# Kernel tuning notes

Measured on AMD Instinct MI355X. Metric: run time of the kernel, lower is better.

Reference implementation:

```python
import jax, jax.numpy as jnp
import numpy as np

B, C, E = 4, 2048, 1024
H = 16
HD = E // H  # 64

def setup_inputs() -> dict:
    key = jax.random.key(0)
    k1, k2, k3 = jax.random.split(key, 3)
    x = jax.random.normal(k1, (B, C, E), dtype=jnp.float32)
    W_attn = jax.random.normal(k2, (E, 3 * E), dtype=jnp.float32) * 0.02
    W_proj = jax.random.normal(k3, (E, E), dtype=jnp.float32) * 0.02
    return {"x": x, "W_attn": W_attn, "W_proj": W_proj}

def reference(x, W_attn, W_proj):
    b, c, e = x.shape
    qkv = x @ W_attn                      # [B,C,3E]
    q, k, v = jnp.split(qkv, 3, axis=-1)
    # [B,C,E] -> [B,H,C,HD]
    q = q.reshape(b, c, H, HD).transpose(0, 2, 1, 3)
    k = k.reshape(b, c, H, HD).transpose(0, 2, 1, 3)
    v = v.reshape(b, c, H, HD).transpose(0, 2, 1, 3)
    scale = 1.0 / np.sqrt(HD).astype(np.float32)
    att = jnp.einsum('bhqd,bhkd->bhqk', q, k) * scale  # [B,H,C,C]
    causal = jnp.tril(jnp.ones((c, c), dtype=bool))
    att = jnp.where(causal[None, None, :, :], att, -jnp.inf)
    att = jax.nn.softmax(att, axis=-1)
    y = jnp.einsum('bhqk,bhkd->bhqd', att, v)          # [B,H,C,HD]
    y = y.transpose(0, 2, 1, 3).reshape(b, c, e)
    return y @ W_proj
```

## Files before the change

kernel.cpp:

```cpp
#include <hip/hip_runtime.h>
#include <hip/hip_bf16.h>


typedef unsigned short ushort_t;
typedef __attribute__((ext_vector_type(8))) short short8;
typedef __attribute__((ext_vector_type(4))) float floatx4;
typedef __attribute__((ext_vector_type(16))) float floatx16;
typedef __attribute__((ext_vector_type(2))) unsigned uintx2;

#define NH   16
#define SEQ  2048
#define EMB  1024
#define HDIM 64

#define MFMA32(a, b, c) __builtin_amdgcn_mfma_f32_32x32x16_bf16(a, b, c, 0, 0, 0)
#define WAITVM4() asm volatile("s_waitcnt vmcnt(4)" ::: "memory")
#define WAITVM0() asm volatile("s_waitcnt vmcnt(0)" ::: "memory")

__device__ __forceinline__ ushort_t f2bf(float f) {
    union { float f; unsigned u; } v; v.f = f;
    unsigned r = (v.u + 0x7fffu + ((v.u >> 16) & 1u)) >> 16;
    return (ushort_t)r;
}

__device__ __forceinline__ unsigned cvtpk(float lo, float hi) {
    unsigned r;
    asm("v_cvt_pk_bf16_f32 %0, %1, %2" : "=v"(r) : "v"(lo), "v"(hi));
    return r;
}

__device__ __forceinline__ uintx2 pl32(unsigned a, unsigned b) {
    return __builtin_amdgcn_permlane32_swap(a, b, false, false);
}

__device__ __forceinline__ short8 mk8(unsigned a, unsigned b, unsigned c, unsigned d) {
    union { unsigned w[4]; short8 s; } t;
    t.w[0] = a; t.w[1] = b; t.w[2] = c; t.w[3] = d;
    return t.s;
}

#if defined(__has_builtin) && __has_builtin(__builtin_amdgcn_global_load_lds)
#define HAS_GLL 1
__device__ __forceinline__ void gload16(const ushort_t* g, ushort_t* l) {
    __builtin_amdgcn_global_load_lds((const __attribute__((address_space(1))) void*)g,
                                     (__attribute__((address_space(3))) void*)l, 16, 0, 0);
}
#else
#define HAS_GLL 0
#endif

__global__ __launch_bounds__(256) void cast_k(const float* __restrict__ in,
                                              ushort_t* __restrict__ out) {
    int i = blockIdx.x * 256 + threadIdx.x;
    float4 v0 = ((const float4*)in)[i * 2];
    float4 v1 = ((const float4*)in)[i * 2 + 1];
    short8 t;
    t[0] = (short)f2bf(v0.x); t[1] = (short)f2bf(v0.y);
    t[2] = (short)f2bf(v0.z); t[3] = (short)f2bf(v0.w);
    t[4] = (short)f2bf(v1.x); t[5] = (short)f2bf(v1.y);
    t[6] = (short)f2bf(v1.z); t[7] = (short)f2bf(v1.w);
    ((short8*)out)[i] = t;
}

__global__ void transpose_cast_k(const float* __restrict__ in, ushort_t* __restrict__ out,
                                 int R, int Cc) {
    __shared__ ushort_t tile[32][33];
    int x  = blockIdx.x * 32 + threadIdx.x;
    int y0 = blockIdx.y * 32;
#pragma unroll
    for (int i = 0; i < 32; i += 8)
        tile[threadIdx.y + i][threadIdx.x] = f2bf(in[(size_t)(y0 + threadIdx.y + i) * Cc + x]);
    __syncthreads();
    int xo = blockIdx.y * 32 + threadIdx.x;
    int yo = blockIdx.x * 32;
#pragma unroll
    for (int i = 0; i < 32; i += 8)
        out[(size_t)(yo + threadIdx.y + i) * R + xo] = tile[threadIdx.x][threadIdx.y + i];
}

__global__ void transpose_v_k(const ushort_t* __restrict__ in, ushort_t* __restrict__ out) {
    __shared__ ushort_t tile[32][33];
    int bh = blockIdx.z;
    int c0 = blockIdx.x * 32, d0 = blockIdx.y * 32;
#pragma unroll
    for (int i = 0; i < 32; i += 8)
        tile[threadIdx.y + i][threadIdx.x] =
            in[((size_t)bh * SEQ + c0 + threadIdx.y + i) * HDIM + d0 + threadIdx.x];
    __syncthreads();
#pragma unroll
    for (int i = 0; i < 32; i += 8)
        out[((size_t)bh * HDIM + d0 + threadIdx.y + i) * SEQ + c0 + threadIdx.x] =
            tile[threadIdx.x][threadIdx.y + i];
}

template<int EPI>
__global__ __launch_bounds__(256) void gemm_bt(const ushort_t* __restrict__ A,
                                               const ushort_t* __restrict__ Bt,
                                               void* __restrict__ O0v,
                                               ushort_t* __restrict__ O1,
                                               ushort_t* __restrict__ O2,
                                               int M, int N, int K) {
    __shared__ __align__(16) ushort_t SMg[2 * 128 * 64];
    ushort_t* As = SMg;
    ushort_t* Bs = SMg + 128 * 64;
    const int tid  = threadIdx.x;
    const int wv   = tid >> 6, lane = tid & 63, quad = lane >> 4, l15 = lane & 15;
    const int wm   = wv >> 1, wn = wv & 1;
    const int bm   = blockIdx.x, bn = blockIdx.y;
    const int lrow = lane >> 3;
    const int kg   = (lane & 7) ^ (lrow & 7);
    const int sw   = l15 & 7;
    const float qsc = (EPI == 1 && bn < 8) ? 0.18033688011112042f : 1.0f;

    floatx4 acc[4][4];
#pragma unroll
    for (int i = 0; i < 4; i++)
#pragma unroll
        for (int j = 0; j < 4; j++) acc[i][j] = (floatx4){0.f, 0.f, 0.f, 0.f};

    for (int kt = 0; kt < K; kt += 64) {
#pragma unroll
        for (int it = 0; it < 4; it++) {
            int r0 = it * 32 + wv * 8;
            const ushort_t* ga = &A [(size_t)(bm * 128 + r0 + lrow) * K + kt + kg * 8];
            const ushort_t* gb = &Bt[(size_t)(bn * 128 + r0 + lrow) * K + kt + kg * 8];
#if HAS_GLL
            gload16(ga, &As[r0 * 64]);
            gload16(gb, &Bs[r0 * 64]);
#else
            *(uint4*)&As[(r0 + lrow) * 64 + (lane & 7) * 8] = *(const uint4*)ga;
            *(uint4*)&Bs[(r0 + lrow) * 64 + (lane & 7) * 8] = *(const uint4*)gb;
#endif
        }
        __syncthreads();
#pragma unroll
        for (int ks = 0; ks < 2; ks++) {
            short8 af[4], bf[4];
#pragma unroll
            for (int i = 0; i < 4; i++)
                af[i] = *(const short8*)&As[(wm * 64 + i * 16 + l15) * 64 + (((ks * 4 + quad) ^ sw) * 8)];
#pragma unroll
            for (int j = 0; j < 4; j++)
                bf[j] = *(const short8*)&Bs[(wn * 64 + j * 16 + l15) * 64 + (((ks * 4 + quad) ^ sw) * 8)];
#pragma unroll
            for (int i = 0; i < 4; i++)
#pragma unroll
                for (int j = 0; j < 4; j++)
                    acc[i][j] = __builtin_amdgcn_mfma_f32_16x16x32_bf16(af[i], bf[j], acc[i][j], 0, 0, 0);
        }
        __syncthreads();
    }

    if (EPI == 0) {
#pragma unroll
        for (int i = 0; i < 4; i++)
#pragma unroll
            for (int j = 0; j < 4; j++)
#pragma unroll
                for (int r = 0; r < 4; r++) {
                    int row = bm * 128 + wm * 64 + i * 16 + quad * 4 + r;
                    int col = bn * 128 + wn * 64 + j * 16 + l15;
                    ((float*)O0v)[(size_t)row * N + col] = acc[i][j][r];
                }
    } else {
        ushort_t* E = SMg;
#pragma unroll
        for (int i = 0; i < 4; i++)
#pragma unroll
            for (int j = 0; j < 4; j++)
#pragma unroll
                for (int r = 0; r < 4; r++) {
                    int lr = wm * 64 + i * 16 + quad * 4 + r;
                    int lc = wn * 64 + j * 16 + l15;
                    E[lr * 128 + (((lc >> 3) ^ (lr & 7)) << 3) + (lc & 7)] =
                        f2bf(acc[i][j][r] * qsc);
                }
        __syncthreads();
#pragma unroll
        for (int k2 = 0; k2 < 8; k2++) {
            int id   = wv * 512 + k2 * 64 + lane;
            int head = id >> 10;
            int lr   = (id >> 3) & 127;
            int g    = id & 7;
            int gg   = (head * 8 + g) ^ (lr & 7);
            uint4 val = *(const uint4*)&E[lr * 128 + gg * 8];
            int row = bm * 128 + lr;
            int col = bn * 128 + head * 64;
            int b = row >> 11, c = row & 2047;
            int which = col >> 10, nn = col & 1023;
            int hh = nn >> 6;
            ushort_t* dst = (which == 0) ? (ushort_t*)O0v : (which == 1) ? O1 : O2;
            *(uint4*)&dst[((size_t)(b * NH + hh) * SEQ + c) * HDIM + g * 8] = val;
        }
    }
}

__device__ __forceinline__ void stage_kv(const ushort_t* __restrict__ Kg,
                                         const ushort_t* __restrict__ Vtg,
                                         ushort_t* Kn, ushort_t* Vn,
                                         int bh, int j, int wv, int lane) {
    const int lrow = lane >> 3;
    const int kgs  = (lane & 7) ^ (lrow & 7);
#pragma unroll
    for (int it = 0; it < 2; it++) {
        int r0 = it * 32 + wv * 8;
        const ushort_t* gk = &Kg [((size_t)bh * SEQ  + j * 64 + r0 + lrow) * HDIM + kgs * 8];
        const ushort_t* gv = &Vtg[((size_t)bh * HDIM + r0 + lrow) * SEQ + j * 64 + kgs * 8];
#if HAS_GLL
        gload16(gk, &Kn[r0 * 64]);
        gload16(gv, &Vn[r0 * 64]);
#else
        *(uint4*)&Kn[(r0 + lrow) * 64 + (lane & 7) * 8] = *(const uint4*)gk;
        *(uint4*)&Vn[(r0 + lrow) * 64 + (lane & 7) * 8] = *(const uint4*)gv;
#endif
    }
}

__global__ __launch_bounds__(256) void attn3_k(const ushort_t* __restrict__ Qg,
                                               const ushort_t* __restrict__ Kg,
                                               const ushort_t* __restrict__ Vtg,
                                               ushort_t* __restrict__ Y) {
    __shared__ __align__(16) ushort_t SM[3 * 8192];
    const int tid  = threadIdx.x;
    const int wv   = tid >> 6, lane = tid & 63;
    const int l31  = lane & 31, hf = lane >> 5;
    const int bh   = blockIdx.x, z = blockIdx.y;
    const int qs7  = l31 & 7;
    const int b = bh >> 4, hh = bh & 15;

    for (int pp = 0; pp < 2; pp++) {
        const int qb = pp ? (15 - z) : z;
        const int qrow0 = qb * 128 + wv * 32;
        const int q_abs = qrow0 + l31;
        const int jmax_w = 2 * qb + (wv >> 1);
        const int nj = 2 * qb + 2;

        short8 qf[4];
        {
            const ushort_t* qp = Qg + ((size_t)bh * SEQ + q_abs) * HDIM + hf * 8;
#pragma unroll
            for (int ks = 0; ks < 4; ks++) qf[ks] = *(const short8*)(qp + ks * 16);
        }

        floatx16 o0, o1;
#pragma unroll
        for (int r = 0; r < 16; r++) { o0[r] = 0.f; o1[r] = 0.f; }
        float l_i = 0.f;

        stage_kv(Kg, Vtg, SM,        SM + 4096,  bh, 0, wv, lane);
        stage_kv(Kg, Vtg, SM + 8192, SM + 12288, bh, 1, wv, lane);
        WAITVM4();
        __builtin_amdgcn_s_barrier();

        int cur = 0, stg = 2;
        for (int j = 0; j < nj; j++) {
            ushort_t* Ks = SM + cur * 8192;
            ushort_t* Vs = Ks + 4096;

            const bool issue = (j + 2 < nj);
            if (issue) {
                ushort_t* Kn = SM + stg * 8192;
                stage_kv(Kg, Vtg, Kn, Kn + 4096, bh, j + 2, wv, lane);
            }

            if (j <= jmax_w) {
                floatx16 s0, s1;
#pragma unroll
                for (int r = 0; r < 16; r++) { s0[r] = 0.f; s1[r] = 0.f; }
                __builtin_amdgcn_s_setprio(1);
#pragma unroll
                for (int ks = 0; ks < 4; ks++) {
                    int slot = ((hf + 2 * ks) ^ qs7) * 8;
                    short8 k0 = *(const short8*)&Ks[l31 * 64 + slot];
                    short8 k1 = *(const short8*)&Ks[(32 + l31) * 64 + slot];
                    s0 = MFMA32(k0, qf[ks], s0);
                    s1 = MFMA32(k1, qf[ks], s1);
                }
                __builtin_amdgcn_s_setprio(0);

                if (j == jmax_w) {
                    const int kb0 = j * 64 + 4 * hf;
#pragma unroll
                    for (int r = 0; r < 16; r++) {
                        int key = kb0 + (r & 3) + 8 * (r >> 2);
                        if (key > q_abs)      s0[r] = -1e30f;
                        if (key + 32 > q_abs) s1[r] = -1e30f;
                    }
                }

                float rs0 = 0.f, rs1 = 0.f;
#pragma unroll
                for (int r = 0; r < 16; r++) {
                    s0[r] = __builtin_amdgcn_exp2f(s0[r]);
                    s1[r] = __builtin_amdgcn_exp2f(s1[r]);
                    rs0 += s0[r]; rs1 += s1[r];
                }
                float rs = rs0 + rs1;
                rs += __shfl_xor(rs, 32);
                l_i += rs;

                unsigned u0[8], u1[8];
#pragma unroll
                for (int g = 0; g < 4; g++) {
                    u0[2 * g]     = cvtpk(s0[4 * g],     s0[4 * g + 1]);
                    u0[2 * g + 1] = cvtpk(s0[4 * g + 2], s0[4 * g + 3]);
                    u1[2 * g]     = cvtpk(s1[4 * g],     s1[4 * g + 1]);
                    u1[2 * g + 1] = cvtpk(s1[4 * g + 2], s1[4 * g + 3]);
                }
                unsigned pw[16];
#pragma unroll
                for (int t = 0; t < 2; t++) {
                    const unsigned* u = t ? u1 : u0;
#pragma unroll
                    for (int p = 0; p < 2; p++) {
#pragma unroll
                        for (int i = 0; i < 2; i++) {
                            uintx2 r = pl32(u[4 * p + i], u[4 * p + 2 + i]);
                            pw[8 * t + 4 * p + i]     = r[0];
                            pw[8 * t + 4 * p + 2 + i] = r[1];
                        }
                    }
                }

                __builtin_amdgcn_s_setprio(1);
#pragma unroll
                for (int ks = 0; ks < 4; ks++) {
                    int slot = ((hf + 2 * ks) ^ qs7) * 8;
                    short8 v0 = *(const short8*)&Vs[l31 * 64 + slot];
                    short8 v1 = *(const short8*)&Vs[(32 + l31) * 64 + slot];
                    short8 pf = mk8(pw[4 * ks], pw[4 * ks + 1], pw[4 * ks + 2], pw[4 * ks + 3]);
                    o0 = MFMA32(v0, pf, o0);
                    o1 = MFMA32(v1, pf, o1);
                }
                __builtin_amdgcn_s_setprio(0);
            }

            if (issue) { WAITVM4(); } else { WAITVM0(); }
            __builtin_amdgcn_s_barrier();
            cur = (cur == 2) ? 0 : cur + 1;
            stg = (stg == 2) ? 0 : stg + 1;
        }

        ushort_t* Ew = SM + wv * 2048;
        float inv = 1.0f / l_i;
#pragma unroll
        for (int g = 0; g < 4; g++) {
            uint2 w0, w1;
            w0.x = cvtpk(o0[g * 4] * inv,     o0[g * 4 + 1] * inv);
            w0.y = cvtpk(o0[g * 4 + 2] * inv, o0[g * 4 + 3] * inv);
            w1.x = cvtpk(o1[g * 4] * inv,     o1[g * 4 + 1] * inv);
            w1.y = cvtpk(o1[g * 4 + 2] * inv, o1[g * 4 + 3] * inv);
            *(uint2*)&Ew[l31 * 64 + ((g       ^ qs7) * 8) + 4 * hf] = w0;
            *(uint2*)&Ew[l31 * 64 + (((4 + g) ^ qs7) * 8) + 4 * hf] = w1;
        }
        const int dg = lane & 7;
#pragma unroll
        for (int sb = 0; sb < 4; sb++) {
            int ql = sb * 8 + (lane >> 3);
            uint4 v = *(const uint4*)&Ew[ql * 64 + ((dg ^ (ql & 7)) * 8)];
            *(uint4*)&Y[((size_t)(b * SEQ + qrow0 + ql)) * EMB + hh * HDIM + dg * 8] = v;
        }
        __syncthreads();
    }
}

extern "C" void kernel_launch(void* const* d_in, const int* in_sizes, int n_in,
                              void* d_out, int out_size, void* d_ws, size_t ws_size,
                              hipStream_t stream) {
    const float* x      = (const float*)d_in[0];
    const float* W_attn = (const float*)d_in[1];
    const float* W_proj = (const float*)d_in[2];

    char* ws = (char*)d_ws;
    ushort_t* Wt_attn = (ushort_t*)(ws);
    ushort_t* Wt_proj = (ushort_t*)(ws + 6291456);
    ushort_t* Xb      = (ushort_t*)(ws + 8388608);
    ushort_t* Vt      = Xb;
    ushort_t* Qb      = (ushort_t*)(ws + 25165824);
    ushort_t* Kb      = (ushort_t*)(ws + 41943040);
    ushort_t* Vb      = (ushort_t*)(ws + 58720256);
    ushort_t* Yb      = Vb;

    cast_k<<<4096, 256, 0, stream>>>(x, Xb);
    transpose_cast_k<<<dim3(3072 / 32, 1024 / 32), dim3(32, 8), 0, stream>>>(W_attn, Wt_attn, 1024, 3072);
    transpose_cast_k<<<dim3(1024 / 32, 1024 / 32), dim3(32, 8), 0, stream>>>(W_proj, Wt_proj, 1024, 1024);
    gemm_bt<1><<<dim3(8192 / 128, 3072 / 128), 256, 0, stream>>>(Xb, Wt_attn, Qb, Kb, Vb, 8192, 3072, 1024);
    transpose_v_k<<<dim3(SEQ / 32, HDIM / 32, 64), dim3(32, 8), 0, stream>>>(Vb, Vt);
    attn3_k<<<dim3(64, 8), 256, 0, stream>>>(Qb, Kb, Vt, Yb);
    gemm_bt<0><<<dim3(8192 / 128, 1024 / 128), 256, 0, stream>>>(Yb, Wt_proj, d_out,
                                                                 nullptr, nullptr, 8192, 1024, 1024);
}
```

Measured before the change: 254.6 us.

## Rewrite QKV GEMM with 256x256 double-buffered tiles and fuse V transpose

Replaces the templated QKV GEMM with a dedicated 512-thread kernel. It uses 256x256 output tiles, double-buffered LDS staging interleaved with MFMA phases, and a swizzled block order meant to improve L2 reuse. The epilogue writes V directly in transposed layout, which removes the separate transpose_v_k launch and its extra global round trip. In exchange it uses 128KB of shared memory per block, a larger accumulator footprint, and a gathered scalar LDS read pattern for the V transpose that may be bank-conflicted.

Result: slower. 268.4 us (+5.4%).

```diff
diff --git a/kernel.cpp b/kernel.cpp
--- a/kernel.cpp
+++ b/kernel.cpp
@@ -14,7 +14,9 @@
 #define HDIM 64
 
 #define MFMA32(a, b, c) __builtin_amdgcn_mfma_f32_32x32x16_bf16(a, b, c, 0, 0, 0)
+#define MFMA16(a, b, c) __builtin_amdgcn_mfma_f32_16x16x32_bf16(a, b, c, 0, 0, 0)
 #define WAITVM4() asm volatile("s_waitcnt vmcnt(4)" ::: "memory")
+#define WAITVM2() asm volatile("s_waitcnt vmcnt(2)" ::: "memory")
 #define WAITVM0() asm volatile("s_waitcnt vmcnt(0)" ::: "memory")
 
 __device__ __forceinline__ ushort_t f2bf(float f) {
@@ -47,6 +49,10 @@
 }
 #else
 #define HAS_GLL 0
+__device__ __forceinline__ void gload16(const ushort_t* g, ushort_t* l) {
+    int lane = threadIdx.x & 63;
+    *(uint4*)(l + lane * 8) = *(const uint4*)g;
+}
 #endif
 
 __global__ __launch_bounds__(256) void cast_k(const float* __restrict__ in,
@@ -78,31 +84,183 @@
         out[(size_t)(yo + threadIdx.y + i) * R + xo] = tile[threadIdx.x][threadIdx.y + i];
 }
 
-__global__ void transpose_v_k(const ushort_t* __restrict__ in, ushort_t* __restrict__ out) {
-    __shared__ ushort_t tile[32][33];
-    int bh = blockIdx.z;
-    int c0 = blockIdx.x * 32, d0 = blockIdx.y * 32;
-#pragma unroll
-    for (int i = 0; i < 32; i += 8)
-        tile[threadIdx.y + i][threadIdx.x] =
-            in[((size_t)bh * SEQ + c0 + threadIdx.y + i) * HDIM + d0 + threadIdx.x];
+__global__ __launch_bounds__(512, 2) void gemm_qkv_k(const ushort_t* __restrict__ A,
+                                                     const ushort_t* __restrict__ Bt,
+                                                     ushort_t* __restrict__ Qo,
+                                                     ushort_t* __restrict__ Ko,
+                                                     ushort_t* __restrict__ Vto) {
+    __shared__ __align__(16) ushort_t SM[65536];
+    const int tid  = threadIdx.x;
+    const int wv   = tid >> 6, lane = tid & 63;
+    const int wm   = wv >> 2, wn = wv & 3;
+    const int quad = lane >> 4, l15 = lane & 15, sw = l15 & 7;
+    const int lrow = lane >> 3;
+    const int kg   = (lane & 7) ^ lrow;
+
+    int bid = (int)blockIdx.x;
+    bid = (bid & 7) * 48 + (bid >> 3);
+    const int bm = bid / 12, bn = bid % 12;
+
+    const size_t abase = (size_t)bm * 256 * 1024;
+    const size_t bbase = (size_t)bn * 256 * 1024;
+
+    floatx4 acc[8][4];
+#pragma unroll
+    for (int i = 0; i < 8; i++)
+#pragma unroll
+        for (int j = 0; j < 4; j++) acc[i][j] = (floatx4){0.f, 0.f, 0.f, 0.f};
+
+    const int brB  = wn * 64 + wm * 32;
+    const int brA1 = wm * 128 + wn * 16;
+    const int brA2 = brA1 + 64;
+
+#define STA(buf, t, rb) gload16(&A [abase + (size_t)((rb) + lrow) * 1024 + (t) * 64 + kg * 8], \
+                                &SM[(buf) * 32768 + (rb) * 64])
+#define STB(buf, t, rb) gload16(&Bt[bbase + (size_t)((rb) + lrow) * 1024 + (t) * 64 + kg * 8], \
+                                &SM[(buf) * 32768 + 16384 + (rb) * 64])
+
+    STB(0, 0, brB);  STB(0, 0, brB + 8);  STB(0, 0, brB + 16); STB(0, 0, brB + 24);
+    STA(0, 0, brA1); STA(0, 0, brA1 + 8); STA(0, 0, brA2);     STA(0, 0, brA2 + 8);
+    WAITVM0();
+    __builtin_amdgcn_s_barrier();
+
+    for (int t = 0; t < 16; t++) {
+        const int cb = t & 1, nb = cb ^ 1;
+        const ushort_t* As = &SM[cb * 32768];
+        const ushort_t* Bs = &SM[cb * 32768 + 16384];
+        const bool st = (t < 15);
+        short8 af[4][2], bf[4][2];
+
+#pragma unroll
+        for (int i = 0; i < 4; i++)
+#pragma unroll
+            for (int ks = 0; ks < 2; ks++)
+                af[i][ks] = *(const short8*)&As[(wm * 128 + i * 16 + l15) * 64 + (((ks * 4 + quad) ^ sw) * 8)];
+#pragma unroll
+        for (int j = 0; j < 2; j++)
+#pragma unroll
+            for (int ks = 0; ks < 2; ks++)
+                bf[j][ks] = *(const short8*)&Bs[(wn * 64 + j * 16 + l15) * 64 + (((ks * 4 + quad) ^ sw) * 8)];
+        if (st) { STB(nb, t + 1, brB); STB(nb, t + 1, brB + 8); }
+        __builtin_amdgcn_s_setprio(1);
+#pragma unroll
+        for (int i = 0; i < 4; i++)
+#pragma unroll
+            for (int j = 0; j < 2; j++)
+#pragma unroll
+                for (int ks = 0; ks < 2; ks++)
+                    acc[i][j] = MFMA16(af[i][ks], bf[j][ks], acc[i][j]);
+        __builtin_amdgcn_s_setprio(0);
+        __builtin_amdgcn_s_barrier();
+
+#pragma unroll
+        for (int j = 2; j < 4; j++)
+#pragma unroll
+            for (int ks = 0; ks < 2; ks++)
+                bf[j][ks] = *(const short8*)&Bs[(wn * 64 + j * 16 + l15) * 64 + (((ks * 4 + quad) ^ sw) * 8)];
+        if (st) { STB(nb, t + 1, brB + 16); STB(nb, t + 1, brB + 24); }
+        __builtin_amdgcn_s_setprio(1);
+#pragma unroll
+        for (int i = 0; i < 4; i++)
+#pragma unroll
+            for (int j = 2; j < 4; j++)
+#pragma unroll
+                for (int ks = 0; ks < 2; ks++)
+                    acc[i][j] = MFMA16(af[i][ks], bf[j][ks], acc[i][j]);
+        __builtin_amdgcn_s_setprio(0);
+        if (t == 15) { WAITVM0(); } else { WAITVM4(); }
+        __builtin_amdgcn_s_barrier();
+
+#pragma unroll
+        for (int i = 0; i < 4; i++)
+#pragma unroll
+            for (int ks = 0; ks < 2; ks++)
+                af[i][ks] = *(const short8*)&As[(wm * 128 + 64 + i * 16 + l15) * 64 + (((ks * 4 + quad) ^ sw) * 8)];
+        if (st) { STA(nb, t + 1, brA1); STA(nb, t + 1, brA1 + 8); }
+        __builtin_amdgcn_s_setprio(1);
+#pragma unroll
+        for (int i = 0; i < 4; i++)
+#pragma unroll
+            for (int j = 0; j < 2; j++)
+#pragma unroll
+                for (int ks = 0; ks < 2; ks++)
+                    acc[i + 4][j] = MFMA16(af[i][ks], bf[j][ks], acc[i + 4][j]);
+        __builtin_amdgcn_s_setprio(0);
+        __builtin_amdgcn_s_barrier();
+
+        if (st) { STA(nb, t + 1, brA2); STA(nb, t + 1, brA2 + 8); }
+        __builtin_amdgcn_s_setprio(1);
+#pragma unroll
+        for (int i = 0; i < 4; i++)
+#pragma unroll
+            for (int j = 2; j < 4; j++)
+#pragma unroll
+                for (int ks = 0; ks < 2; ks++)
+                    acc[i + 4][j] = MFMA16(af[i][ks], bf[j][ks], acc[i + 4][j]);
+        __builtin_amdgcn_s_setprio(0);
+        if (st) { WAITVM2(); }
+        __builtin_amdgcn_s_barrier();
+    }
+#undef STA
+#undef STB
+
     __syncthreads();
-#pragma unroll
-    for (int i = 0; i < 32; i += 8)
-        out[((size_t)bh * HDIM + d0 + threadIdx.y + i) * SEQ + c0 + threadIdx.x] =
-            tile[threadIdx.x][threadIdx.y + i];
-}
-
-template<int EPI>
-__global__ __launch_bounds__(256) void gemm_bt(const ushort_t* __restrict__ A,
-                                               const ushort_t* __restrict__ Bt,
-                                               void* __restrict__ O0v,
-                                               ushort_t* __restrict__ O1,
-                                               ushort_t* __restrict__ O2,
-                                               int M, int N, int K) {
-    __shared__ __align__(16) ushort_t SMg[2 * 128 * 64];
-    ushort_t* As = SMg;
-    ushort_t* Bs = SMg + 128 * 64;
+    ushort_t* E = SM;
+    const float qsc = (bn < 4) ? 0.18033688011112042f : 1.0f;
+#pragma unroll
+    for (int i = 0; i < 8; i++)
+#pragma unroll
+        for (int j = 0; j < 4; j++)
+#pragma unroll
+            for (int r = 0; r < 4; r++) {
+                int lr = wm * 128 + i * 16 + quad * 4 + r;
+                int lc = wn * 64 + j * 16 + l15;
+                E[lr * 256 + (((lc >> 3) ^ (lr & 31)) << 3) + (lc & 7)] =
+                    f2bf(acc[i][j][r] * qsc);
+            }
+    __syncthreads();
+
+    if (bn < 8) {
+        ushort_t* dst0 = (bn < 4) ? Qo : Ko;
+#pragma unroll
+        for (int it = 0; it < 16; it++) {
+            int id   = it * 512 + tid;
+            int g    = id & 7;
+            int hcol = (id >> 3) & 3;
+            int lr   = id >> 5;
+            uint4 val = *(const uint4*)&E[lr * 256 + (((hcol * 8 + g) ^ (lr & 31)) << 3)];
+            int row = bm * 256 + lr;
+            int b = row >> 11, c = row & 2047;
+            int hh = ((bn & 3) * 4 + hcol);
+            *(uint4*)&dst0[((size_t)(b * NH + hh) * SEQ + c) * HDIM + g * 8] = val;
+        }
+    } else {
+        int b = bm >> 3;
+#pragma unroll
+        for (int it = 0; it < 16; it++) {
+            int id   = it * 512 + tid;
+            int drow = id >> 5;
+            int cseg = id & 31;
+            int hcol = drow >> 6, d = drow & 63;
+            ushort_t tmp[8];
+#pragma unroll
+            for (int k = 0; k < 8; k++) {
+                int c = cseg * 8 + k;
+                tmp[k] = E[c * 256 + (((drow >> 3) ^ (c & 31)) << 3) + (drow & 7)];
+            }
+            int cglob = (bm & 7) * 256 + cseg * 8;
+            int hh = (bn & 3) * 4 + hcol;
+            *(uint4*)&Vto[((size_t)(b * NH + hh) * HDIM + d) * SEQ + cglob] = *(const uint4*)tmp;
+        }
+    }
+}
+
+__global__ __launch_bounds__(256) void gemm_proj_k(const ushort_t* __restrict__ A,
+                                                   const ushort_t* __restrict__ Bt,
+                                                   float* __restrict__ O,
+                                                   int M, int N, int K) {
+    __shared__ __align__(16) ushort_t As[128 * 64];
+    __shared__ __align__(16) ushort_t Bs[128 * 64];
     const int tid  = threadIdx.x;
     const int wv   = tid >> 6, lane = tid & 63, quad = lane >> 4, l15 = lane & 15;
     const int wm   = wv >> 1, wn = wv & 1;
@@ -110,7 +268,6 @@
     const int lrow = lane >> 3;
     const int kg   = (lane & 7) ^ (lrow & 7);
     const int sw   = l15 & 7;
-    const float qsc = (EPI == 1 && bn < 8) ? 0.18033688011112042f : 1.0f;
 
     floatx4 acc[4][4];
 #pragma unroll
@@ -124,13 +281,8 @@
             int r0 = it * 32 + wv * 8;
             const ushort_t* ga = &A [(size_t)(bm * 128 + r0 + lrow) * K + kt + kg * 8];
             const ushort_t* gb = &Bt[(size_t)(bn * 128 + r0 + lrow) * K + kt + kg * 8];
-#if HAS_GLL
             gload16(ga, &As[r0 * 64]);
             gload16(gb, &Bs[r0 * 64]);
-#else
-            *(uint4*)&As[(r0 + lrow) * 64 + (lane & 7) * 8] = *(const uint4*)ga;
-            *(uint4*)&Bs[(r0 + lrow) * 64 + (lane & 7) * 8] = *(const uint4*)gb;
-#endif
         }
         __syncthreads();
 #pragma unroll
@@ -146,53 +298,21 @@
             for (int i = 0; i < 4; i++)
 #pragma unroll
                 for (int j = 0; j < 4; j++)
-                    acc[i][j] = __builtin_amdgcn_mfma_f32_16x16x32_bf16(af[i], bf[j], acc[i][j], 0, 0, 0);
+                    acc[i][j] = MFMA16(af[i], bf[j], acc[i][j]);
         }
         __syncthreads();
     }
 
-    if (EPI == 0) {
-#pragma unroll
-        for (int i = 0; i < 4; i++)
-#pragma unroll
-            for (int j = 0; j < 4; j++)
-#pragma unroll
-                for (int r = 0; r < 4; r++) {
-                    int row = bm * 128 + wm * 64 + i * 16 + quad * 4 + r;
-                    int col = bn * 128 + wn * 64 + j * 16 + l15;
-                    ((float*)O0v)[(size_t)row * N + col] = acc[i][j][r];
-                }
-    } else {
-        ushort_t* E = SMg;
-#pragma unroll
-        for (int i = 0; i < 4; i++)
-#pragma unroll
-            for (int j = 0; j < 4; j++)
-#pragma unroll
-                for (int r = 0; r < 4; r++) {
-                    int lr = wm * 64 + i * 16 + quad * 4 + r;
-                    int lc = wn * 64 + j * 16 + l15;
-                    E[lr * 128 + (((lc >> 3) ^ (lr & 7)) << 3) + (lc & 7)] =
-                        f2bf(acc[i][j][r] * qsc);
-                }
-        __syncthreads();
-#pragma unroll
-        for (int k2 = 0; k2 < 8; k2++) {
-            int id   = wv * 512 + k2 * 64 + lane;
-            int head = id >> 10;
-            int lr   = (id >> 3) & 127;
-            int g    = id & 7;
-            int gg   = (head * 8 + g) ^ (lr & 7);
-            uint4 val = *(const uint4*)&E[lr * 128 + gg * 8];
-            int row = bm * 128 + lr;
-            int col = bn * 128 + head * 64;
-            int b = row >> 11, c = row & 2047;
-            int which = col >> 10, nn = col & 1023;
-            int hh = nn >> 6;
-            ushort_t* dst = (which == 0) ? (ushort_t*)O0v : (which == 1) ? O1 : O2;
-            *(uint4*)&dst[((size_t)(b * NH + hh) * SEQ + c) * HDIM + g * 8] = val;
-        }
-    }
+#pragma unroll
+    for (int i = 0; i < 4; i++)
+#pragma unroll
+        for (int j = 0; j < 4; j++)
+#pragma unroll
+            for (int r = 0; r < 4; r++) {
+                int row = bm * 128 + wm * 64 + i * 16 + quad * 4 + r;
+                int col = bn * 128 + wn * 64 + j * 16 + l15;
+                O[(size_t)row * N + col] = acc[i][j][r];
+            }
 }
 
 __device__ __forceinline__ void stage_kv(const ushort_t* __restrict__ Kg,
@@ -206,13 +326,8 @@
         int r0 = it * 32 + wv * 8;
         const ushort_t* gk = &Kg [((size_t)bh * SEQ  + j * 64 + r0 + lrow) * HDIM + kgs * 8];
         const ushort_t* gv = &Vtg[((size_t)bh * HDIM + r0 + lrow) * SEQ + j * 64 + kgs * 8];
-#if HAS_GLL
         gload16(gk, &Kn[r0 * 64]);
         gload16(gv, &Vn[r0 * 64]);
-#else
-        *(uint4*)&Kn[(r0 + lrow) * 64 + (lane & 7) * 8] = *(const uint4*)gk;
-        *(uint4*)&Vn[(r0 + lrow) * 64 + (lane & 7) * 8] = *(const uint4*)gv;
-#endif
     }
 }
 
@@ -302,22 +417,22 @@
                 unsigned u0[8], u1[8];
 #pragma unroll
                 for (int g = 0; g < 4; g++) {
-                    u0[2 * g]     = cvtpk(s0[4 * g],     s0[4 * g + 1]);
-                    u0[2 * g + 1] = cvtpk(s0[4 * g + 2], s0[4 * g + 3]);
-                    u1[2 * g]     = cvtpk(s1[4 * g],     s1[4 * g + 1]);
-                    u1[2 * g + 1] = cvtpk(s1[4 * g + 2], s1[4 * g + 3]);
+                    u0[2 * g]     = cvtpk(s0[g * 4],     s0[g * 4 + 1]);
+                    u0[2 * g + 1] = cvtpk(s0[g * 4 + 2], s0[g * 4 + 3]);
+                    u1[2 * g]     = cvtpk(s1[g * 4],     s1[g * 4 + 1]);
+                    u1[2 * g + 1] = cvtpk(s1[g * 4 + 2], s1[g * 4 + 3]);
                 }
                 unsigned pw[16];
 #pragma unroll
-                for (int t = 0; t < 2; t++) {
-                    const unsigned* u = t ? u1 : u0;
+                for (int tt = 0; tt < 2; tt++) {
+                    const unsigned* u = tt ? u1 : u0;
 #pragma unroll
                     for (int p = 0; p < 2; p++) {
 #pragma unroll
                         for (int i = 0; i < 2; i++) {
                             uintx2 r = pl32(u[4 * p + i], u[4 * p + 2 + i]);
-                            pw[8 * t + 4 * p + i]     = r[0];
-                            pw[8 * t + 4 * p + 2 + i] = r[1];
+                            pw[8 * tt + 4 * p + i]     = r[0];
+                            pw[8 * tt + 4 * p + 2 + i] = r[1];
                         }
                     }
                 }
@@ -375,18 +490,16 @@
     ushort_t* Wt_attn = (ushort_t*)(ws);
     ushort_t* Wt_proj = (ushort_t*)(ws + 6291456);
     ushort_t* Xb      = (ushort_t*)(ws + 8388608);
-    ushort_t* Vt      = Xb;
+    ushort_t* Yb      = Xb;
     ushort_t* Qb      = (ushort_t*)(ws + 25165824);
     ushort_t* Kb      = (ushort_t*)(ws + 41943040);
-    ushort_t* Vb      = (ushort_t*)(ws + 58720256);
-    ushort_t* Yb      = Vb;
+    ushort_t* Vt      = (ushort_t*)(ws + 58720256);
 
     cast_k<<<4096, 256, 0, stream>>>(x, Xb);
     transpose_cast_k<<<dim3(3072 / 32, 1024 / 32), dim3(32, 8), 0, stream>>>(W_attn, Wt_attn, 1024, 3072);
     transpose_cast_k<<<dim3(1024 / 32, 1024 / 32), dim3(32, 8), 0, stream>>>(W_proj, Wt_proj, 1024, 1024);
-    gemm_bt<1><<<dim3(8192 / 128, 3072 / 128), 256, 0, stream>>>(Xb, Wt_attn, Qb, Kb, Vb, 8192, 3072, 1024);
-    transpose_v_k<<<dim3(SEQ / 32, HDIM / 32, 64), dim3(32, 8), 0, stream>>>(Vb, Vt);
+    gemm_qkv_k<<<384, 512, 0, stream>>>(Xb, Wt_attn, Qb, Kb, Vt);
     attn3_k<<<dim3(64, 8), 256, 0, stream>>>(Qb, Kb, Vt, Yb);
-    gemm_bt<0><<<dim3(8192 / 128, 1024 / 128), 256, 0, stream>>>(Yb, Wt_proj, d_out,
-                                                                 nullptr, nullptr, 8192, 1024, 1024);
-}
+    gemm_proj_k<<<dim3(8192 / 128, 1024 / 128), 256, 0, stream>>>(Yb, Wt_proj, (float*)d_out,
+                                                                  8192, 1024, 1024);
+}
```

## Fuse V transpose into QKV GEMM epilogue and fold Q scale into weights

Applied to the files above, without the earlier changes.

The QKV GEMM epilogue now writes V directly in transposed [B,H,D,C] layout, so the separate transpose_v_k launch and its extra read and write of V are gone. The softmax scale for Q is folded into the W_attn transpose-cast, which removes a multiply from the epilogue. The LDS-staged coalesced epilogue is replaced by direct scattered stores (2-byte stores for Q/K, 8-byte for V), which may hurt store coalescing. Buffer aliasing is also reshuffled.

New measurement: 245.2 us. 3.7% less time.

```diff
diff --git a/kernel.cpp b/kernel.cpp
--- a/kernel.cpp
+++ b/kernel.cpp
@@ -14,6 +14,7 @@
 #define HDIM 64
 
 #define MFMA32(a, b, c) __builtin_amdgcn_mfma_f32_32x32x16_bf16(a, b, c, 0, 0, 0)
+#define MFMA16(a, b, c) __builtin_amdgcn_mfma_f32_16x16x32_bf16(a, b, c, 0, 0, 0)
 #define WAITVM4() asm volatile("s_waitcnt vmcnt(4)" ::: "memory")
 #define WAITVM0() asm volatile("s_waitcnt vmcnt(0)" ::: "memory")
 
@@ -63,34 +64,20 @@
 }
 
 __global__ void transpose_cast_k(const float* __restrict__ in, ushort_t* __restrict__ out,
-                                 int R, int Cc) {
+                                 int R, int Cc, float sc, int ncut) {
     __shared__ ushort_t tile[32][33];
     int x  = blockIdx.x * 32 + threadIdx.x;
     int y0 = blockIdx.y * 32;
+    float s = (x < ncut) ? sc : 1.0f;
 #pragma unroll
     for (int i = 0; i < 32; i += 8)
-        tile[threadIdx.y + i][threadIdx.x] = f2bf(in[(size_t)(y0 + threadIdx.y + i) * Cc + x]);
+        tile[threadIdx.y + i][threadIdx.x] = f2bf(in[(size_t)(y0 + threadIdx.y + i) * Cc + x] * s);
     __syncthreads();
     int xo = blockIdx.y * 32 + threadIdx.x;
     int yo = blockIdx.x * 32;
 #pragma unroll
     for (int i = 0; i < 32; i += 8)
         out[(size_t)(yo + threadIdx.y + i) * R + xo] = tile[threadIdx.x][threadIdx.y + i];
-}
-
-__global__ void transpose_v_k(const ushort_t* __restrict__ in, ushort_t* __restrict__ out) {
-    __shared__ ushort_t tile[32][33];
-    int bh = blockIdx.z;
-    int c0 = blockIdx.x * 32, d0 = blockIdx.y * 32;
-#pragma unroll
-    for (int i = 0; i < 32; i += 8)
-        tile[threadIdx.y + i][threadIdx.x] =
-            in[((size_t)bh * SEQ + c0 + threadIdx.y + i) * HDIM + d0 + threadIdx.x];
-    __syncthreads();
-#pragma unroll
-    for (int i = 0; i < 32; i += 8)
-        out[((size_t)bh * HDIM + d0 + threadIdx.y + i) * SEQ + c0 + threadIdx.x] =
-            tile[threadIdx.x][threadIdx.y + i];
 }
 
 template<int EPI>
@@ -100,9 +87,8 @@
                                                ushort_t* __restrict__ O1,
                                                ushort_t* __restrict__ O2,
                                                int M, int N, int K) {
-    __shared__ __align__(16) ushort_t SMg[2 * 128 * 64];
-    ushort_t* As = SMg;
-    ushort_t* Bs = SMg + 128 * 64;
+    __shared__ __align__(16) ushort_t As[128 * 64];
+    __shared__ __align__(16) ushort_t Bs[128 * 64];
     const int tid  = threadIdx.x;
     const int wv   = tid >> 6, lane = tid & 63, quad = lane >> 4, l15 = lane & 15;
     const int wm   = wv >> 1, wn = wv & 1;
@@ -110,7 +96,6 @@
     const int lrow = lane >> 3;
     const int kg   = (lane & 7) ^ (lrow & 7);
     const int sw   = l15 & 7;
-    const float qsc = (EPI == 1 && bn < 8) ? 0.18033688011112042f : 1.0f;
 
     floatx4 acc[4][4];
 #pragma unroll
@@ -146,7 +131,7 @@
             for (int i = 0; i < 4; i++)
 #pragma unroll
                 for (int j = 0; j < 4; j++)
-                    acc[i][j] = __builtin_amdgcn_mfma_f32_16x16x32_bf16(af[i], bf[j], acc[i][j], 0, 0, 0);
+                    acc[i][j] = MFMA16(af[i], bf[j], acc[i][j]);
         }
         __syncthreads();
     }
@@ -163,35 +148,28 @@
                     ((float*)O0v)[(size_t)row * N + col] = acc[i][j][r];
                 }
     } else {
-        ushort_t* E = SMg;
 #pragma unroll
         for (int i = 0; i < 4; i++)
 #pragma unroll
-            for (int j = 0; j < 4; j++)
-#pragma unroll
-                for (int r = 0; r < 4; r++) {
-                    int lr = wm * 64 + i * 16 + quad * 4 + r;
-                    int lc = wn * 64 + j * 16 + l15;
-                    E[lr * 128 + (((lc >> 3) ^ (lr & 7)) << 3) + (lc & 7)] =
-                        f2bf(acc[i][j][r] * qsc);
-                }
-        __syncthreads();
-#pragma unroll
-        for (int k2 = 0; k2 < 8; k2++) {
-            int id   = wv * 512 + k2 * 64 + lane;
-            int head = id >> 10;
-            int lr   = (id >> 3) & 127;
-            int g    = id & 7;
-            int gg   = (head * 8 + g) ^ (lr & 7);
-            uint4 val = *(const uint4*)&E[lr * 128 + gg * 8];
-            int row = bm * 128 + lr;
-            int col = bn * 128 + head * 64;
-            int b = row >> 11, c = row & 2047;
-            int which = col >> 10, nn = col & 1023;
-            int hh = nn >> 6;
-            ushort_t* dst = (which == 0) ? (ushort_t*)O0v : (which == 1) ? O1 : O2;
-            *(uint4*)&dst[((size_t)(b * NH + hh) * SEQ + c) * HDIM + g * 8] = val;
-        }
+            for (int j = 0; j < 4; j++) {
+                int row0 = bm * 128 + wm * 64 + i * 16 + quad * 4;
+                int col  = bn * 128 + wn * 64 + j * 16 + l15;
+                int b = row0 >> 11;
+                int which = col >> 10, nn = col & 1023;
+                int hh = nn >> 6, d = nn & 63;
+                if (which == 2) {
+                    uint2 pv;
+                    pv.x = cvtpk(acc[i][j][0], acc[i][j][1]);
+                    pv.y = cvtpk(acc[i][j][2], acc[i][j][3]);
+                    *(uint2*)&O2[((size_t)(b * NH + hh) * HDIM + d) * SEQ + (row0 & 2047)] = pv;
+                } else {
+                    ushort_t* dst = (which == 0) ? (ushort_t*)O0v : O1;
+#pragma unroll
+                    for (int r = 0; r < 4; r++)
+                        dst[((size_t)(b * NH + hh) * SEQ + ((row0 + r) & 2047)) * HDIM + d] =
+                            f2bf(acc[i][j][r]);
+                }
+            }
     }
 }
 
@@ -302,22 +280,22 @@
                 unsigned u0[8], u1[8];
 #pragma unroll
                 for (int g = 0; g < 4; g++) {
-                    u0[2 * g]     = cvtpk(s0[4 * g],     s0[4 * g + 1]);
-                    u0[2 * g + 1] = cvtpk(s0[4 * g + 2], s0[4 * g + 3]);
-                    u1[2 * g]     = cvtpk(s1[4 * g],     s1[4 * g + 1]);
-                    u1[2 * g + 1] = cvtpk(s1[4 * g + 2], s1[4 * g + 3]);
+                    u0[2 * g]     = cvtpk(s0[g * 4],     s0[g * 4 + 1]);
+                    u0[2 * g + 1] = cvtpk(s0[g * 4 + 2], s0[g * 4 + 3]);
+                    u1[2 * g]     = cvtpk(s1[g * 4],     s1[g * 4 + 1]);
+                    u1[2 * g + 1] = cvtpk(s1[g * 4 + 2], s1[g * 4 + 3]);
                 }
                 unsigned pw[16];
 #pragma unroll
-                for (int t = 0; t < 2; t++) {
-                    const unsigned* u = t ? u1 : u0;
+                for (int tt = 0; tt < 2; tt++) {
+                    const unsigned* u = tt ? u1 : u0;
 #pragma unroll
                     for (int p = 0; p < 2; p++) {
 #pragma unroll
                         for (int i = 0; i < 2; i++) {
                             uintx2 r = pl32(u[4 * p + i], u[4 * p + 2 + i]);
-                            pw[8 * t + 4 * p + i]     = r[0];
-                            pw[8 * t + 4 * p + 2 + i] = r[1];
+                            pw[8 * tt + 4 * p + i]     = r[0];
+                            pw[8 * tt + 4 * p + 2 + i] = r[1];
                         }
                     }
                 }
@@ -375,18 +353,21 @@
     ushort_t* Wt_attn = (ushort_t*)(ws);
     ushort_t* Wt_proj = (ushort_t*)(ws + 6291456);
     ushort_t* Xb      = (ushort_t*)(ws + 8388608);
-    ushort_t* Vt      = Xb;
+    ushort_t* Yb      = Xb;
     ushort_t* Qb      = (ushort_t*)(ws + 25165824);
     ushort_t* Kb      = (ushort_t*)(ws + 41943040);
-    ushort_t* Vb      = (ushort_t*)(ws + 58720256);
-    ushort_t* Yb      = Vb;
+    ushort_t* Vt      = (ushort_t*)(ws + 58720256);
+
+    const float c2 = 0.18033688011112042f;
 
     cast_k<<<4096, 256, 0, stream>>>(x, Xb);
-    transpose_cast_k<<<dim3(3072 / 32, 1024 / 32), dim3(32, 8), 0, stream>>>(W_attn, Wt_attn, 1024, 3072);
-    transpose_cast_k<<<dim3(1024 / 32, 1024 / 32), dim3(32, 8), 0, stream>>>(W_proj, Wt_proj, 1024, 1024);
-    gemm_bt<1><<<dim3(8192 / 128, 3072 / 128), 256, 0, stream>>>(Xb, Wt_attn, Qb, Kb, Vb, 8192, 3072, 1024);
-    transpose_v_k<<<dim3(SEQ / 32, HDIM / 32, 64), dim3(32, 8), 0, stream>>>(Vb, Vt);
+    transpose_cast_k<<<dim3(3072 / 32, 1024 / 32), dim3(32, 8), 0, stream>>>(W_attn, Wt_attn,
+                                                                             1024, 3072, c2, 1024);
+    transpose_cast_k<<<dim3(1024 / 32, 1024 / 32), dim3(32, 8), 0, stream>>>(W_proj, Wt_proj,
+                                                                             1024, 1024, 1.0f, 0);
+    gemm_bt<1><<<dim3(8192 / 128, 3072 / 128), 256, 0, stream>>>(Xb, Wt_attn, Qb, Kb, Vt,
+                                                                 8192, 3072, 1024);
     attn3_k<<<dim3(64, 8), 256, 0, stream>>>(Qb, Kb, Vt, Yb);
-    gemm_bt<0><<<dim3(8192 / 128, 1024 / 128), 256, 0, stream>>>(Yb, Wt_proj, d_out,
+    gemm_bt<0><<<dim3(8192 / 128, 1024 / 128), 256, 0, stream>>>(Yb, Wt_proj, (float*)d_out,
                                                                  nullptr, nullptr, 8192, 1024, 1024);
 }
```
